# Kernel tuning notes

Measured on AMD Instinct MI355X. Metric: run time of the kernel, lower is better.

The kernel has to match this reference:

```python
import jax, jax.numpy as jnp
import numpy as np

H = 4            # heads
C = 64           # per-head dim (= hidden, PyG TransformerConv semantics)
HD = 64          # hidden_dim
L = 2            # num_layers
NT = 2           # node types: 0=task, 1=machine
ET = ((0, 1), (1, 0))  # edge types: (src_nt, dst_nt)
N = 16384        # nodes per type (== max_nodes -> simple pos-enc slice)
E = 262144       # edges per edge type


def _ln(x, g, b):
    mu = x.mean(-1, keepdims=True)
    var = ((x - mu) ** 2).mean(-1, keepdims=True)
    return (x - mu) * jax.lax.rsqrt(var + 1e-5) * g + b


def _tconv(x_src, x_dst, ei, Wq, bq, Wk, bk, Wv, bv, Ws, bs, Wb):
    # PyG TransformerConv: heads=H, out_channels=C, concat=False, beta=True
    n_dst = x_dst.shape[0]
    src, dst = ei[0], ei[1]
    q = (x_dst @ Wq + bq).reshape(-1, H, C)
    k = (x_src @ Wk + bk).reshape(-1, H, C)
    v = (x_src @ Wv + bv).reshape(-1, H, C)
    logits = jnp.einsum('ehc,ehc->eh', q[dst], k[src]) * (1.0 / float(np.sqrt(C)))  # [E,H]
    m = jax.ops.segment_max(logits, dst, num_segments=n_dst)          # [N,H] segment softmax
    ex = jnp.exp(logits - m[dst])
    denom = jax.ops.segment_sum(ex, dst, num_segments=n_dst)
    alpha = ex / denom[dst]                                            # [E,H]
    msg = (alpha[:, :, None] * v[src]).reshape(-1, H * C)              # [E,H*C]
    out = jax.ops.segment_sum(msg, dst, num_segments=n_dst)
    out = out.reshape(n_dst, H, C).mean(axis=1)                        # concat=False -> head mean
    r = x_dst @ Ws + bs                                                # lin_skip
    beta = jax.nn.sigmoid(jnp.concatenate([out, r, out - r], -1) @ Wb) # lin_beta, [N,1]
    return beta * r + (1.0 - beta) * out


def _forward(edge_index, x, W_in, b_in, type_emb, pos, Wq, bq, Wk, bk, Wv, bv,
             Wskip, bskip, Wbeta, ln_g, ln_b, ff_W1, ff_b1, ff_W2, ff_b2, W_out, b_out):
    # input proj + type embedding + positional encoding (num_nodes == max_nodes -> slice)
    h = [x[t] @ W_in[t] + b_in[t] + type_emb[t] + pos[t] for t in range(NT)]
    for l in range(L):
        hn = [jnp.zeros_like(h[0]), jnp.zeros_like(h[1])]
        for e, (s, d) in enumerate(ET):  # HeteroConv, aggr='sum'
            hn[d] = hn[d] + _tconv(h[s], h[d], edge_index[e],
                                   Wq[l, e], bq[l, e], Wk[l, e], bk[l, e],
                                   Wv[l, e], bv[l, e], Wskip[l, e], bskip[l, e], Wbeta[l, e])
        for t in range(NT):
            hr = _ln(h[t] + hn[t], ln_g[l, t], ln_b[l, t])
            ff = jax.nn.gelu(hr @ ff_W1[l, t] + ff_b1[l, t], approximate=False) @ ff_W2[l, t] + ff_b2[l, t]
            h[t] = hr + ff
    return jnp.stack([h[t] @ W_out[t] + b_out[t] for t in range(NT)])  # [NT,N,HD]


def setup_inputs() -> dict:
    key = jax.random.key(0)
    ks = jax.random.split(key, 16)
    w = lambda k, s: 0.02 * jax.random.normal(k, s, jnp.float32)
    NE = len(ET)
    return {
        'x': jax.random.normal(ks[0], (NT, N, HD), jnp.float32),
        'edge_index': jax.random.randint(ks[1], (NE, 2, E), 0, N, jnp.int32),
        'W_in': w(ks[2], (NT, HD, HD)), 'b_in': jnp.zeros((NT, HD), jnp.float32),
        'type_emb': w(ks[3], (NT, HD)),
        'pos': w(ks[4], (NT, N, HD)),
        'Wq': w(ks[5], (L, NE, HD, H * C)), 'bq': jnp.zeros((L, NE, H * C), jnp.float32),
        'Wk': w(ks[6], (L, NE, HD, H * C)), 'bk': jnp.zeros((L, NE, H * C), jnp.float32),
        'Wv': w(ks[7], (L, NE, HD, H * C)), 'bv': jnp.zeros((L, NE, H * C), jnp.float32),
        'Wskip': w(ks[8], (L, NE, HD, HD)), 'bskip': jnp.zeros((L, NE, HD), jnp.float32),
        'Wbeta': w(ks[9], (L, NE, 3 * HD, 1)),
        'ln_g': jnp.ones((L, NT, HD), jnp.float32), 'ln_b': jnp.zeros((L, NT, HD), jnp.float32),
        'ff_W1': w(ks[10], (L, NT, HD, 4 * HD)), 'ff_b1': jnp.zeros((L, NT, 4 * HD), jnp.float32),
        'ff_W2': w(ks[11], (L, NT, 4 * HD, HD)), 'ff_b2': jnp.zeros((L, NT, HD), jnp.float32),
        'W_out': w(ks[12], (NT, HD, HD)), 'b_out': jnp.zeros((NT, HD), jnp.float32),
    }


def reference(x, edge_index, W_in, b_in, type_emb, pos, Wq, bq, Wk, bk, Wv, bv,
              Wskip, bskip, Wbeta, ln_g, ln_b, ff_W1, ff_b1, ff_W2, ff_b2, W_out, b_out):
    return _forward(edge_index, x, W_in, b_in, type_emb, pos, Wq, bq, Wk, bk, Wv, bv,
                    Wskip, bskip, Wbeta, ln_g, ln_b, ff_W1, ff_b1, ff_W2, ff_b2, W_out, b_out)
```

## Files before the change

### kernel.cpp

```cpp
#include <hip/hip_runtime.h>
#include <math.h>

#define NN 16384
#define EE 262144

typedef __bf16 v8bf __attribute__((ext_vector_type(8)));
typedef __bf16 v4bf __attribute__((ext_vector_type(4)));
typedef float  v4f  __attribute__((ext_vector_type(4)));
typedef float  v2f  __attribute__((ext_vector_type(2)));

#define OFF_CNT     0
#define OFF_FILL    (2*NN)
#define OFF_ROWPTR  (4*NN)
#define OFF_COLSRC  98816
#define OFF_H       623104
#define OFF_HN      (OFF_H  + 2*NN*64)
#define OFF_Q       (OFF_HN + 2*NN*64)
#define OFF_KV      (OFF_Q  + 2*NN*128)
#define OFF_R       (OFF_KV + 2*NN*128)

__device__ __forceinline__ float blo(unsigned u) { return __uint_as_float(u << 16); }
__device__ __forceinline__ float bhi(unsigned u) { return __uint_as_float(u & 0xffff0000u); }
__device__ __forceinline__ unsigned short f2b(float f) {
  __bf16 h = (__bf16)f;
  return *(unsigned short*)&h;
}

__global__ void count_kernel(const int* __restrict__ ei, int* __restrict__ cnt) {
  int idx = blockIdx.x * 256 + threadIdx.x;
  if (idx >= 2 * EE) return;
  int et = idx >> 18;
  int j  = idx & (EE - 1);
  int dst = ei[et * 2 * EE + EE + j];
  atomicAdd(&cnt[et * NN + dst], 1);
}

__global__ __launch_bounds__(1024) void scan_kernel(const int* __restrict__ cnt,
                                                    int* __restrict__ rowptr,
                                                    int* __restrict__ fill) {
  int et = blockIdx.x;
  const int* c = cnt + et * NN;
  __shared__ int sums[1024];
  int tid = threadIdx.x;
  int base = tid * 16;
  int loc[16];
  int s = 0;
#pragma unroll
  for (int i = 0; i < 16; ++i) { loc[i] = s; s += c[base + i]; }
  sums[tid] = s;
  __syncthreads();
  for (int off = 1; off < 1024; off <<= 1) {
    int v = 0;
    if (tid >= off) v = sums[tid - off];
    __syncthreads();
    if (tid >= off) sums[tid] += v;
    __syncthreads();
  }
  int ebase = (tid == 0) ? 0 : sums[tid - 1];
  int* rp = rowptr + et * (NN + 1);
  int* fl = fill + et * NN;
#pragma unroll
  for (int i = 0; i < 16; ++i) {
    rp[base + i] = ebase + loc[i];
    fl[base + i] = ebase + loc[i];
  }
  if (tid == 1023) rp[NN] = sums[1023];
}

__global__ void scatter_kernel(const int* __restrict__ ei, int* __restrict__ fill,
                               int* __restrict__ colsrc) {
  int idx = blockIdx.x * 256 + threadIdx.x;
  if (idx >= 2 * EE) return;
  int et = idx >> 18;
  int j  = idx & (EE - 1);
  int src = ei[et * 2 * EE + j];
  int dst = ei[et * 2 * EE + EE + j];
  int pos = atomicAdd(&fill[et * NN + dst], 1);
  colsrc[et * EE + pos] = (et * NN + src) << 9;
}

struct GemmDesc {
  const float *A, *B, *bias, *bias2, *add;
  char* C;
  int Ncols, Cld, ntiles, gelu, otype;
};
struct GemmPack { GemmDesc d[8]; int nd; };

#define LDA 72

__global__ __launch_bounds__(256) void gemm_mfma(GemmPack p) {
  GemmDesc g = p.d[blockIdx.y];
  const int row0 = blockIdx.x * 128;
  const int tid = threadIdx.x;
  const int w = tid >> 6, lane = tid & 63;
  const int l16 = lane & 15, quad = lane >> 4;

  __shared__ __bf16 As[128 * LDA];
  __shared__ __bf16 Bs[64 * LDA];

#pragma unroll
  for (int it = 0; it < 8; ++it) {
    int fi = it * 256 + tid;
    int grow = fi >> 4;
    int kq = (fi & 15) << 2;
    float4 a = *(const float4*)(g.A + (size_t)(row0 + grow) * 64 + kq);
    v4bf c = { (__bf16)a.x, (__bf16)a.y, (__bf16)a.z, (__bf16)a.w };
    *(v4bf*)&As[grow * LDA + kq] = c;
  }

  for (int ct0 = 0; ct0 < g.ntiles; ++ct0) {
    const int col0 = ct0 * 64;
    __syncthreads();
#pragma unroll
    for (int it = 0; it < 4; ++it) {
      int fi = it * 256 + tid;
      int kk = fi >> 4;
      int nq = (fi & 15) << 2;
      float4 b = *(const float4*)(g.B + (size_t)kk * g.Ncols + col0 + nq);
      Bs[(nq + 0) * LDA + kk] = (__bf16)b.x;
      Bs[(nq + 1) * LDA + kk] = (__bf16)b.y;
      Bs[(nq + 2) * LDA + kk] = (__bf16)b.z;
      Bs[(nq + 3) * LDA + kk] = (__bf16)b.w;
    }
    __syncthreads();

    v4f acc[2][4];
#pragma unroll
    for (int rt = 0; rt < 2; ++rt)
#pragma unroll
      for (int ct = 0; ct < 4; ++ct)
#pragma unroll
        for (int r = 0; r < 4; ++r) acc[rt][ct][r] = 0.f;

#pragma unroll
    for (int ks = 0; ks < 2; ++ks) {
      v8bf a0 = *(v8bf*)&As[(w * 32 + l16) * LDA + ks * 32 + quad * 8];
      v8bf a1 = *(v8bf*)&As[(w * 32 + 16 + l16) * LDA + ks * 32 + quad * 8];
#pragma unroll
      for (int ct = 0; ct < 4; ++ct) {
        v8bf bb = *(v8bf*)&Bs[(ct * 16 + l16) * LDA + ks * 32 + quad * 8];
        acc[0][ct] = __builtin_amdgcn_mfma_f32_16x16x32_bf16(a0, bb, acc[0][ct], 0, 0, 0);
        acc[1][ct] = __builtin_amdgcn_mfma_f32_16x16x32_bf16(a1, bb, acc[1][ct], 0, 0, 0);
      }
    }

    float bias_c[4];
#pragma unroll
    for (int ct = 0; ct < 4; ++ct) {
      int col = col0 + ct * 16 + l16;
      float b = g.bias ? g.bias[col] : 0.f;
      if (g.bias2) b += g.bias2[col];
      bias_c[ct] = b;
    }
#pragma unroll
    for (int rt = 0; rt < 2; ++rt)
#pragma unroll
      for (int r = 0; r < 4; ++r) {
        size_t row = row0 + w * 32 + rt * 16 + quad * 4 + r;
        char* cp = g.C + row * (size_t)g.Cld;
#pragma unroll
        for (int ct = 0; ct < 4; ++ct) {
          int col = col0 + ct * 16 + l16;
          float v = acc[rt][ct][r] + bias_c[ct];
          if (g.add) v += g.add[row * g.Ncols + col];
          if (g.gelu) v = 0.5f * v * (1.f + erff(v * 0.70710678118654752f));
          if (g.otype == 0)      *(float*)(cp + col * 4) = v;
          else if (g.otype == 1) *(unsigned short*)(cp + col * 2) = f2b(v);
          else {
            unsigned pk = __builtin_amdgcn_cvt_pk_fp8_f32(v, v, 0, false);
            *(unsigned char*)(cp + col) = (unsigned char)(pk & 0xff);
          }
        }
      }
  }
}

struct FFPack {
  const float *HN, *W1, *b1, *W2, *b2;
  float* H;
  const float *Wout, *bout;
  float* outbuf;
};

__global__ __launch_bounds__(256) void ff_fused(FFPack p) {
  const int t = blockIdx.y;
  const int row0 = blockIdx.x * 64;
  const int tid = threadIdx.x;
  const int w = tid >> 6, lane = tid & 63;
  const int l16 = lane & 15, quad = lane >> 4;

  const float* A  = p.HN + ((size_t)t * NN) * 64;
  const float* W1 = p.W1 + (size_t)t * 64 * 256;
  const float* b1 = p.b1 + t * 256;
  const float* W2 = p.W2 + (size_t)t * 256 * 64;
  const float* b2 = p.b2 + t * 64;

  __shared__ __bf16 As[64 * LDA];
  __shared__ __bf16 A2[64 * LDA];
  __shared__ __bf16 B1s[64 * LDA];
  __shared__ __bf16 B2s[64 * LDA];

#pragma unroll
  for (int it = 0; it < 4; ++it) {
    int fi = it * 256 + tid;
    int grow = fi >> 4;
    int kq = (fi & 15) << 2;
    float4 a = *(const float4*)(A + (size_t)(row0 + grow) * 64 + kq);
    v4bf c = { (__bf16)a.x, (__bf16)a.y, (__bf16)a.z, (__bf16)a.w };
    *(v4bf*)&As[grow * LDA + kq] = c;
  }

  v4f acc2[4];
#pragma unroll
  for (int ct = 0; ct < 4; ++ct)
#pragma unroll
    for (int r = 0; r < 4; ++r) acc2[ct][r] = 0.f;

  for (int c1 = 0; c1 < 4; ++c1) {
#pragma unroll
    for (int it = 0; it < 4; ++it) {
      int fi = it * 256 + tid;
      int kk = fi >> 4;
      int nq = (fi & 15) << 2;
      float4 b = *(const float4*)(W1 + (size_t)kk * 256 + c1 * 64 + nq);
      B1s[(nq + 0) * LDA + kk] = (__bf16)b.x;
      B1s[(nq + 1) * LDA + kk] = (__bf16)b.y;
      B1s[(nq + 2) * LDA + kk] = (__bf16)b.z;
      B1s[(nq + 3) * LDA + kk] = (__bf16)b.w;
      float4 b2v = *(const float4*)(W2 + (size_t)(c1 * 64 + kk) * 64 + nq);
      B2s[(nq + 0) * LDA + kk] = (__bf16)b2v.x;
      B2s[(nq + 1) * LDA + kk] = (__bf16)b2v.y;
      B2s[(nq + 2) * LDA + kk] = (__bf16)b2v.z;
      B2s[(nq + 3) * LDA + kk] = (__bf16)b2v.w;
    }
    __syncthreads();

    v4f acc1[4];
#pragma unroll
    for (int ct = 0; ct < 4; ++ct)
#pragma unroll
      for (int r = 0; r < 4; ++r) acc1[ct][r] = 0.f;
#pragma unroll
    for (int ks = 0; ks < 2; ++ks) {
      v8bf a = *(v8bf*)&As[(w * 16 + l16) * LDA + ks * 32 + quad * 8];
#pragma unroll
      for (int ct = 0; ct < 4; ++ct) {
        v8bf bb = *(v8bf*)&B1s[(ct * 16 + l16) * LDA + ks * 32 + quad * 8];
        acc1[ct] = __builtin_amdgcn_mfma_f32_16x16x32_bf16(a, bb, acc1[ct], 0, 0, 0);
      }
    }
#pragma unroll
    for (int ct = 0; ct < 4; ++ct) {
      float bb = b1[c1 * 64 + ct * 16 + l16];
#pragma unroll
      for (int r = 0; r < 4; ++r) {
        float v = acc1[ct][r] + bb;
        v = 0.5f * v * (1.f + erff(v * 0.70710678118654752f));
        A2[(w * 16 + quad * 4 + r) * LDA + ct * 16 + l16] = (__bf16)v;
      }
    }
#pragma unroll
    for (int ks = 0; ks < 2; ++ks) {
      v8bf a = *(v8bf*)&A2[(w * 16 + l16) * LDA + ks * 32 + quad * 8];
#pragma unroll
      for (int ct = 0; ct < 4; ++ct) {
        v8bf bb = *(v8bf*)&B2s[(ct * 16 + l16) * LDA + ks * 32 + quad * 8];
        acc2[ct] = __builtin_amdgcn_mfma_f32_16x16x32_bf16(a, bb, acc2[ct], 0, 0, 0);
      }
    }
    __syncthreads();
  }

  if (!p.outbuf) {
#pragma unroll
    for (int ct = 0; ct < 4; ++ct) {
      int col = ct * 16 + l16;
      float bb = b2[col];
#pragma unroll
      for (int r = 0; r < 4; ++r) {
        size_t row = (size_t)t * NN + row0 + w * 16 + quad * 4 + r;
        float v = acc2[ct][r] + bb + p.HN[row * 64 + col];
        p.H[row * 64 + col] = v;
      }
    }
    return;
  }

#pragma unroll
  for (int ct = 0; ct < 4; ++ct) {
    int col = ct * 16 + l16;
    float bb = b2[col];
#pragma unroll
    for (int r = 0; r < 4; ++r) {
      int lrow = w * 16 + quad * 4 + r;
      size_t row = (size_t)t * NN + row0 + lrow;
      float v = acc2[ct][r] + bb + p.HN[row * 64 + col];
      A2[lrow * LDA + col] = (__bf16)v;
    }
  }
  {
    const float* Wo = p.Wout + (size_t)t * 64 * 64;
#pragma unroll
    for (int it = 0; it < 4; ++it) {
      int fi = it * 256 + tid;
      int kk = fi >> 4;
      int nq = (fi & 15) << 2;
      float4 b = *(const float4*)(Wo + (size_t)kk * 64 + nq);
      B1s[(nq + 0) * LDA + kk] = (__bf16)b.x;
      B1s[(nq + 1) * LDA + kk] = (__bf16)b.y;
      B1s[(nq + 2) * LDA + kk] = (__bf16)b.z;
      B1s[(nq + 3) * LDA + kk] = (__bf16)b.w;
    }
  }
  __syncthreads();

  v4f acc3[4];
#pragma unroll
  for (int ct = 0; ct < 4; ++ct)
#pragma unroll
    for (int r = 0; r < 4; ++r) acc3[ct][r] = 0.f;
#pragma unroll
  for (int ks = 0; ks < 2; ++ks) {
    v8bf a = *(v8bf*)&A2[(w * 16 + l16) * LDA + ks * 32 + quad * 8];
#pragma unroll
    for (int ct = 0; ct < 4; ++ct) {
      v8bf bb = *(v8bf*)&B1s[(ct * 16 + l16) * LDA + ks * 32 + quad * 8];
      acc3[ct] = __builtin_amdgcn_mfma_f32_16x16x32_bf16(a, bb, acc3[ct], 0, 0, 0);
    }
  }
  const float* bo = p.bout + t * 64;
#pragma unroll
  for (int ct = 0; ct < 4; ++ct) {
    int col = ct * 16 + l16;
    float bb = bo[col];
#pragma unroll
    for (int r = 0; r < 4; ++r) {
      size_t row = (size_t)t * NN + row0 + w * 16 + quad * 4 + r;
      p.outbuf[row * 64 + col] = acc3[ct][r] + bb;
    }
  }
}

struct AggPack {
  const unsigned short *Q;
  const char *KV;
  const float *R;
  const float *Wb;
  const float *Hin;
  const float *lng, *lnb;
  float* outHR;
  const int *rowptr;
  const int *colsrc;
};

__global__ __launch_bounds__(256) void agg_kernel(AggPack p) {
  const int et = blockIdx.y, d = 1 - et;
  int wid = __builtin_amdgcn_readfirstlane(threadIdx.x >> 6);
  int lane = threadIdx.x & 63;
  int node = blockIdx.x * 4 + wid;
  int c4 = lane & 15;
  int cb = ((lane >> 4) << 6) + (c4 << 2);

  const int* rp = p.rowptr + et * (NN + 1);
  const int* cs = p.colsrc + et * EE;
  int start = rp[node], end = rp[node + 1];
  int len = end - start;
  int gnode = d * NN + node;

  uint2 qw = *(const uint2*)(p.Q + ((size_t)gnode << 8) + cb);
  float q0 = blo(qw.x) * 0.125f, q1 = bhi(qw.x) * 0.125f;
  float q2 = blo(qw.y) * 0.125f, q3 = bhi(qw.y) * 0.125f;

  int b[5];
#pragma unroll
  for (int i = 0; i <= 4; ++i) b[i] = start + ((len * i) >> 2);
  float dsum[4] = {0.f, 0.f, 0.f, 0.f};
  float acc[4][4];
#pragma unroll
  for (int s4 = 0; s4 < 4; ++s4)
#pragma unroll
    for (int c = 0; c < 4; ++c) acc[s4][c] = 0.f;

  int maxn = (len + 3) >> 2;
  int last = end - 1;
  for (int it = 0; it < maxn; ++it) {
#pragma unroll
    for (int s4 = 0; s4 < 4; ++s4) {
      int j = b[s4] + it;
      bool act = j < b[s4 + 1];
      int jc = act ? j : last;
      int off = cs[jc];
      const char* rowp = p.KV + off;
      unsigned kw = *(const unsigned*)(rowp + cb);
      unsigned vw = *(const unsigned*)(rowp + 256 + cb);
      v2f kl = __builtin_amdgcn_cvt_pk_f32_fp8((int)kw, false);
      v2f kh = __builtin_amdgcn_cvt_pk_f32_fp8((int)kw, true);
      float pd = q0 * kl[0] + q1 * kl[1] + q2 * kh[0] + q3 * kh[1];
      pd += __shfl_xor(pd, 1);
      pd += __shfl_xor(pd, 2);
      pd += __shfl_xor(pd, 4);
      pd += __shfl_xor(pd, 8);
      float wgt = act ? __expf(pd) : 0.f;
      v2f vl = __builtin_amdgcn_cvt_pk_f32_fp8((int)vw, false);
      v2f vh = __builtin_amdgcn_cvt_pk_f32_fp8((int)vw, true);
      dsum[s4] += wgt;
      acc[s4][0] += wgt * vl[0];
      acc[s4][1] += wgt * vl[1];
      acc[s4][2] += wgt * vh[0];
      acc[s4][3] += wgt * vh[1];
    }
  }
  float dn = (dsum[0] + dsum[1]) + (dsum[2] + dsum[3]);
  float ax = (acc[0][0] + acc[1][0]) + (acc[2][0] + acc[3][0]);
  float ay = (acc[0][1] + acc[1][1]) + (acc[2][1] + acc[3][1]);
  float az = (acc[0][2] + acc[1][2]) + (acc[2][2] + acc[3][2]);
  float aw = (acc[0][3] + acc[1][3]) + (acc[2][3] + acc[3][3]);

  float inv = (len > 0) ? (0.25f / dn) : 0.f;
  float ox = ax * inv, oy = ay * inv, oz = az * inv, ow = aw * inv;
  ox += __shfl_xor(ox, 16); ox += __shfl_xor(ox, 32);
  oy += __shfl_xor(oy, 16); oy += __shfl_xor(oy, 32);
  oz += __shfl_xor(oz, 16); oz += __shfl_xor(oz, 32);
  ow += __shfl_xor(ow, 16); ow += __shfl_xor(ow, 32);

  int cc = c4 << 2;
  float4 r = *(const float4*)(p.R + (size_t)gnode * 64 + cc);
  const float* wb = p.Wb + et * 192;
  float part = ox * wb[cc] + oy * wb[cc + 1] + oz * wb[cc + 2] + ow * wb[cc + 3]
             + r.x * wb[64 + cc] + r.y * wb[64 + cc + 1]
             + r.z * wb[64 + cc + 2] + r.w * wb[64 + cc + 3]
             + (ox - r.x) * wb[128 + cc] + (oy - r.y) * wb[128 + cc + 1]
             + (oz - r.z) * wb[128 + cc + 2] + (ow - r.w) * wb[128 + cc + 3];
  part += __shfl_xor(part, 1);
  part += __shfl_xor(part, 2);
  part += __shfl_xor(part, 4);
  part += __shfl_xor(part, 8);
  float beta = 1.f / (1.f + __expf(-part));

  float4 hv = *(const float4*)(p.Hin + (size_t)gnode * 64 + cc);
  float yx = hv.x + beta * r.x + (1.f - beta) * ox;
  float yy = hv.y + beta * r.y + (1.f - beta) * oy;
  float yz = hv.z + beta * r.z + (1.f - beta) * oz;
  float yw = hv.w + beta * r.w + (1.f - beta) * ow;
  float sa = yx + yy + yz + yw;
  float sb = yx * yx + yy * yy + yz * yz + yw * yw;
  sa += __shfl_xor(sa, 1); sb += __shfl_xor(sb, 1);
  sa += __shfl_xor(sa, 2); sb += __shfl_xor(sb, 2);
  sa += __shfl_xor(sa, 4); sb += __shfl_xor(sb, 4);
  sa += __shfl_xor(sa, 8); sb += __shfl_xor(sb, 8);
  float mu = sa * (1.f / 64.f);
  float var = sb * (1.f / 64.f) - mu * mu;
  float rs = rsqrtf(var + 1e-5f);
  if (lane < 16) {
    const float* lng = p.lng + d * 64;
    const float* lnb = p.lnb + d * 64;
    float4 gg = *(const float4*)(lng + cc);
    float4 bb = *(const float4*)(lnb + cc);
    float4 res;
    res.x = (yx - mu) * rs * gg.x + bb.x;
    res.y = (yy - mu) * rs * gg.y + bb.y;
    res.z = (yz - mu) * rs * gg.z + bb.z;
    res.w = (yw - mu) * rs * gg.w + bb.w;
    *(float4*)(p.outHR + (size_t)gnode * 64 + cc) = res;
  }
}

static void add_desc(GemmPack& p, const float* A, const float* B,
                     const float* bias, const float* bias2, const float* add,
                     void* C, int Nc, int Cld, int gelu, int otype) {
  GemmDesc& g = p.d[p.nd++];
  g.A = A; g.B = B; g.bias = bias; g.bias2 = bias2; g.add = add; g.C = (char*)C;
  g.Ncols = Nc; g.Cld = Cld; g.ntiles = Nc / 64;
  g.gelu = gelu; g.otype = otype;
}

extern "C" void kernel_launch(void* const* d_in, const int* in_sizes, int n_in,
                              void* d_out, int out_size, void* d_ws, size_t ws_size,
                              hipStream_t stream) {
  const float* x        = (const float*)d_in[0];
  const int*   ei       = (const int*)d_in[1];
  const float* W_in     = (const float*)d_in[2];
  const float* b_in     = (const float*)d_in[3];
  const float* type_emb = (const float*)d_in[4];
  const float* pos      = (const float*)d_in[5];
  const float* Wq       = (const float*)d_in[6];
  const float* bq       = (const float*)d_in[7];
  const float* Wk       = (const float*)d_in[8];
  const float* bk       = (const float*)d_in[9];
  const float* Wv       = (const float*)d_in[10];
  const float* bv       = (const float*)d_in[11];
  const float* Wskip    = (const float*)d_in[12];
  const float* bskip    = (const float*)d_in[13];
  const float* Wbeta    = (const float*)d_in[14];
  const float* ln_g     = (const float*)d_in[15];
  const float* ln_b     = (const float*)d_in[16];
  const float* ff_W1    = (const float*)d_in[17];
  const float* ff_b1    = (const float*)d_in[18];
  const float* ff_W2    = (const float*)d_in[19];
  const float* ff_b2    = (const float*)d_in[20];
  const float* W_out    = (const float*)d_in[21];
  const float* b_out    = (const float*)d_in[22];
  float* out = (float*)d_out;

  int*   wsi = (int*)d_ws;
  float* wsf = (float*)d_ws;
  int* cnt    = wsi + OFF_CNT;
  int* fill   = wsi + OFF_FILL;
  int* rowptr = wsi + OFF_ROWPTR;
  int* colsrc = wsi + OFF_COLSRC;
  float* H  = wsf + OFF_H;
  float* HN = wsf + OFF_HN;
  unsigned short* Qb = (unsigned short*)(wsf + OFF_Q);
  char* KVb = (char*)(wsf + OFF_KV);
  float* Rb = wsf + OFF_R;

  hipMemsetAsync(cnt, 0, 2 * NN * sizeof(int), stream);
  count_kernel<<<dim3(2 * EE / 256), dim3(256), 0, stream>>>(ei, cnt);
  scan_kernel<<<dim3(2), dim3(1024), 0, stream>>>(cnt, rowptr, fill);
  scatter_kernel<<<dim3(2 * EE / 256), dim3(256), 0, stream>>>(ei, fill, colsrc);

  {
    GemmPack p{};
    for (int t = 0; t < 2; ++t)
      add_desc(p, x + (size_t)t * NN * 64, W_in + t * 64 * 64,
               b_in + t * 64, type_emb + t * 64, pos + (size_t)t * NN * 64,
               H + (size_t)t * NN * 64, 64, 256, 0, 0);
    gemm_mfma<<<dim3(128, p.nd), dim3(256), 0, stream>>>(p);
  }

  for (int l = 0; l < 2; ++l) {
    {
      GemmPack p{};
      for (int et = 0; et < 2; ++et) {
        int s = et, d = 1 - et;
        int we = l * 2 + et;
        const float* hs = H + (size_t)s * NN * 64;
        const float* hd = H + (size_t)d * NN * 64;
        add_desc(p, hd, Wq + (size_t)we * 64 * 256, bq + we * 256,
                 nullptr, nullptr, (char*)Qb + (size_t)d * NN * 512, 256, 512, 0, 1);
        add_desc(p, hs, Wk + (size_t)we * 64 * 256, bk + we * 256,
                 nullptr, nullptr, KVb + (size_t)s * NN * 512, 256, 512, 0, 2);
        add_desc(p, hs, Wv + (size_t)we * 64 * 256, bv + we * 256,
                 nullptr, nullptr, KVb + (size_t)s * NN * 512 + 256, 256, 512, 0, 2);
        add_desc(p, hd, Wskip + (size_t)we * 64 * 64, bskip + we * 64,
                 nullptr, nullptr, Rb + (size_t)d * NN * 64, 64, 256, 0, 0);
      }
      gemm_mfma<<<dim3(128, p.nd), dim3(256), 0, stream>>>(p);
    }

    AggPack ap;
    ap.Q = Qb; ap.KV = KVb; ap.R = Rb;
    ap.Wb = Wbeta + l * 2 * 192;
    ap.Hin = H;
    ap.lng = ln_g + l * 128;
    ap.lnb = ln_b + l * 128;
    ap.outHR = HN;
    ap.rowptr = rowptr;
    ap.colsrc = colsrc;
    agg_kernel<<<dim3(NN / 4, 2), dim3(256), 0, stream>>>(ap);

    FFPack fp;
    fp.HN = HN;
    fp.W1 = ff_W1 + (size_t)l * 2 * 64 * 256;
    fp.b1 = ff_b1 + l * 2 * 256;
    fp.W2 = ff_W2 + (size_t)l * 2 * 256 * 64;
    fp.b2 = ff_b2 + l * 2 * 64;
    fp.H  = H;
    fp.Wout = W_out;
    fp.bout = b_out;
    fp.outbuf = (l == 1) ? out : nullptr;
    ff_fused<<<dim3(NN / 64, 2), dim3(256), 0, stream>>>(fp);
  }
}
```

Before: 366.5 us.

## Interleave fp8 K/V per 4 columns and software-prefetch next edge rows

New measurement: 376.7 us. 1.03x slower.

```diff
diff --git a/kernel.cpp b/kernel.cpp
--- a/kernel.cpp
+++ b/kernel.cpp
@@ -168,7 +168,12 @@
           else if (g.otype == 1) *(unsigned short*)(cp + col * 2) = f2b(v);
           else {
             unsigned pk = __builtin_amdgcn_cvt_pk_fp8_f32(v, v, 0, false);
-            *(unsigned char*)(cp + col) = (unsigned char)(pk & 0xff);
+            unsigned char bv = (unsigned char)(pk & 0xff);
+            if (g.otype == 2) *(unsigned char*)(cp + col) = bv;
+            else {
+              int off = ((col >> 2) << 3) + (col & 3) + ((g.otype == 4) ? 4 : 0);
+              *(unsigned char*)(cp + off) = bv;
+            }
           }
         }
       }
@@ -383,16 +388,32 @@
 
   int maxn = (len + 3) >> 2;
   int last = end - 1;
+  int kvoff = cb * 2;
+
+  uint2 cur[4];
+  if (len > 0) {
+#pragma unroll
+    for (int s4 = 0; s4 < 4; ++s4) {
+      int jc = min(b[s4], last);
+      cur[s4] = *(const uint2*)(p.KV + cs[jc] + kvoff);
+    }
+  }
+
   for (int it = 0; it < maxn; ++it) {
+    uint2 nxt[4];
+    bool more = (it + 1 < maxn);
+    if (more) {
+#pragma unroll
+      for (int s4 = 0; s4 < 4; ++s4) {
+        int jc = min(b[s4] + it + 1, last);
+        nxt[s4] = *(const uint2*)(p.KV + cs[jc] + kvoff);
+      }
+    }
 #pragma unroll
     for (int s4 = 0; s4 < 4; ++s4) {
-      int j = b[s4] + it;
-      bool act = j < b[s4 + 1];
-      int jc = act ? j : last;
-      int off = cs[jc];
-      const char* rowp = p.KV + off;
-      unsigned kw = *(const unsigned*)(rowp + cb);
-      unsigned vw = *(const unsigned*)(rowp + 256 + cb);
+      bool act = (b[s4] + it) < b[s4 + 1];
+      unsigned kw = cur[s4].x;
+      unsigned vw = cur[s4].y;
       v2f kl = __builtin_amdgcn_cvt_pk_f32_fp8((int)kw, false);
       v2f kh = __builtin_amdgcn_cvt_pk_f32_fp8((int)kw, true);
       float pd = q0 * kl[0] + q1 * kl[1] + q2 * kh[0] + q3 * kh[1];
@@ -408,6 +429,10 @@
       acc[s4][1] += wgt * vl[1];
       acc[s4][2] += wgt * vh[0];
       acc[s4][3] += wgt * vh[1];
+    }
+    if (more) {
+#pragma unroll
+      for (int s4 = 0; s4 < 4; ++s4) cur[s4] = nxt[s4];
     }
   }
   float dn = (dsum[0] + dsum[1]) + (dsum[2] + dsum[3]);
@@ -539,9 +564,9 @@
         add_desc(p, hd, Wq + (size_t)we * 64 * 256, bq + we * 256,
                  nullptr, nullptr, (char*)Qb + (size_t)d * NN * 512, 256, 512, 0, 1);
         add_desc(p, hs, Wk + (size_t)we * 64 * 256, bk + we * 256,
-                 nullptr, nullptr, KVb + (size_t)s * NN * 512, 256, 512, 0, 2);
+                 nullptr, nullptr, KVb + (size_t)s * NN * 512, 256, 512, 0, 3);
         add_desc(p, hs, Wv + (size_t)we * 64 * 256, bv + we * 256,
-                 nullptr, nullptr, KVb + (size_t)s * NN * 512 + 256, 256, 512, 0, 2);
+                 nullptr, nullptr, KVb + (size_t)s * NN * 512, 256, 512, 0, 4);
         add_desc(p, hd, Wskip + (size_t)we * 64 * 64, bskip + we * 64,
                  nullptr, nullptr, Rb + (size_t)d * NN * 64, 64, 256, 0, 0);
       }
```
